# Kernel tuning notes

Hardware: AMD Instinct MI355X
Metric: run time of the kernel (lower is better)

The kernel has to match this reference:

```python
import jax, jax.numpy as jnp
import numpy as np

B, H, S, D = 2, 12, 2048, 64

def setup_inputs() -> dict:
    key = jax.random.key(0)
    kq, kk, kv = jax.random.split(key, 3)
    Q = jax.random.normal(kq, (B, H, S, D), dtype=jnp.float32)
    K = jax.random.normal(kk, (B, H, S, D), dtype=jnp.float32)
    V = jax.random.normal(kv, (B, H, S, D), dtype=jnp.float32)
    return {"Q": Q, "K": K, "V": V}

def reference(Q, K, V):
    # NOTE: original code scales by sqrt(Q.shape[-2]) (the sequence length),
    # not the head dim — reproduced faithfully.
    scale = 1.0 / np.sqrt(Q.shape[-2]).astype(np.float32)
    scores = jnp.einsum('bhqd,bhkd->bhqk', Q, K) * scale  # [B,H,S,S]
    attn = jax.nn.softmax(scores, axis=-1)
    context = jnp.einsum('bhqk,bhkd->bhqd', attn, V)      # [B,H,S,D]
    # torch .squeeze(-1) only removes the last dim if it is size 1; D=64 so no-op
    return context
```

## Files before the change

### kernel.cpp

```cpp
#include <hip/hip_runtime.h>
#include <hip/hip_bf16.h>
#include <math.h>
#include <stdint.h>

#define BATCH 2
#define NH 12
#define SEQ 2048
#define HD 64
#define TQ 64
#define TK 64
#define NHEADS (BATCH*NH)
#define NIT (SEQ / TK)

typedef short bf16x8 __attribute__((ext_vector_type(8)));
typedef float f32x4 __attribute__((ext_vector_type(4)));
typedef float f32x16 __attribute__((ext_vector_type(16)));
typedef unsigned short us4_t __attribute__((ext_vector_type(4)));
typedef unsigned short us8_t __attribute__((ext_vector_type(8)));
typedef unsigned int u32x4 __attribute__((ext_vector_type(4)));

#if __has_builtin(__builtin_amdgcn_exp2f)
#define EXP2F(x) __builtin_amdgcn_exp2f(x)
#else
#define EXP2F(x) exp2f(x)
#endif

static __device__ __forceinline__ unsigned short f2bf(float f) {
    unsigned int u = __float_as_uint(f);
    u += 0x7fffu + ((u >> 16) & 1u);
    return (unsigned short)(u >> 16);
}

static __device__ __forceinline__ unsigned int pack2bf(float a, float b) {
    __hip_bfloat162 v = __float22bfloat162_rn(float2{a, b});
    return *(unsigned int*)&v;
}

static __device__ __forceinline__ void async_cp16(const void* g, void* l) {
    __builtin_amdgcn_global_load_lds(
        (const __attribute__((address_space(1))) void*)g,
        (__attribute__((address_space(3))) void*)(uintptr_t)l,
        16, 0, 0);
}

static __device__ __forceinline__ int tile_off(int r, int c) {
    int rp  = r >> 1;
    int pos = (((r & 1) << 3) | c) ^ (rp & 15);
    return rp * 128 + pos * 8;
}

__global__ __launch_bounds__(256)
void prep_kv(const float* __restrict__ K, const float* __restrict__ V,
             unsigned short* __restrict__ Kb, unsigned short* __restrict__ Vtb) {
    __shared__ unsigned short T[64][66];
    const int bh = blockIdx.x >> 5;
    const int s0 = (blockIdx.x & 31) * 64;
    const int tid = threadIdx.x;
    const size_t off = ((size_t)bh * SEQ + s0) * HD;

    #pragma unroll
    for (int u = 0; u < 4; ++u) {
        int idx = u * 1024 + tid * 4;
        float4 a = *(const float4*)&K[off + idx];
        us4_t r4 = { f2bf(a.x), f2bf(a.y), f2bf(a.z), f2bf(a.w) };
        *(us4_t*)&Kb[off + idx] = r4;
    }
    #pragma unroll
    for (int u = 0; u < 4; ++u) {
        int idx = u * 1024 + tid * 4;
        int r = idx >> 6, col = idx & 63;
        float4 a = *(const float4*)&V[off + idx];
        *(unsigned int*)&T[r][col]     = pack2bf(a.x, a.y);
        *(unsigned int*)&T[r][col + 2] = pack2bf(a.z, a.w);
    }
    __syncthreads();
    unsigned short* Vdst = Vtb + (size_t)bh * HD * SEQ;
    const int g = tid & 7, dd = tid >> 3;
    #pragma unroll
    for (int h = 0; h < 2; ++h) {
        int d = dd + 32 * h;
        us8_t r8;
        #pragma unroll
        for (int j = 0; j < 8; ++j) {
            int src = ((g >> 1) << 4) + ((j >> 2) << 3) + ((g & 1) << 2) + (j & 3);
            r8[j] = T[src][d];
        }
        *(us8_t*)&Vdst[(size_t)d * SEQ + s0 + g * 8] = r8;
    }
}

__global__ __launch_bounds__(256, 3)
void fa_main(const float* __restrict__ Q,
             const unsigned short* __restrict__ Kb,
             const unsigned short* __restrict__ Vtb,
             float* __restrict__ O, float qs) {
    const int x  = blockIdx.x & 7;
    const int t  = blockIdx.x >> 3;
    const int bh = x + 8 * (t % 3);
    const int qt = t / 3;
    const int q0 = qt * TQ;

    __shared__ __align__(16) unsigned char SH[49664];
    float* Lsum = (float*)(SH + 49152);
    float* Linv = (float*)(SH + 49408);
    float* ORed = (float*)SH;
    unsigned short* QS = (unsigned short*)(SH + 32768);

    const int tid  = threadIdx.x;
    const int w    = tid >> 6;
    const int mt   = w >> 1;
    const int nt   = w & 1;
    const int lane = tid & 63;
    const int l31  = lane & 31;
    const int hi   = lane >> 5;

    const float*          Qh = Q   + ((size_t)bh * SEQ + q0) * HD;
    const unsigned short* Kh = Kb  + (size_t)bh * SEQ * HD;
    const unsigned short* Vh = Vtb + (size_t)bh * HD * SEQ;

    int rS[2], cS[2];
    #pragma unroll
    for (int i = 0; i < 2; ++i) {
        int rp = w * 8 + 4 * i + (lane >> 4);
        int lc = (lane & 15) ^ (rp & 15);
        rS[i] = 2 * rp + (lc >> 3);
        cS[i] = lc & 7;
    }
    const int dst0 = (w * 8 + 0) * 128, dst1 = (w * 8 + 4) * 128;
    const size_t kG0 = (size_t)rS[0] * HD  + cS[0] * 8;
    const size_t kG1 = (size_t)rS[1] * HD  + cS[1] * 8;
    const size_t vG0 = (size_t)rS[0] * SEQ + cS[0] * 8;
    const size_t vG1 = (size_t)rS[1] * SEQ + cS[1] * 8;

    {
        unsigned short* K0 = (unsigned short*)(SH);
        unsigned short* V0 = (unsigned short*)(SH + 8192);
        async_cp16(Kh + kG0, &K0[dst0]);
        async_cp16(Kh + kG1, &K0[dst1]);
        async_cp16(Vh + vG0, &V0[dst0]);
        async_cp16(Vh + vG1, &V0[dst1]);
    }
    #pragma unroll
    for (int u = 0; u < 4; ++u) {
        int idx = u * 1024 + tid * 4;
        int r = idx >> 6, col = idx & 63;
        float4 a = *(const float4*)&Qh[idx];
        uint2 pk = { pack2bf(a.x * qs, a.y * qs), pack2bf(a.z * qs, a.w * qs) };
        *(uint2*)&QS[tile_off(r, col >> 3) + (col & 7)] = pk;
    }
    __syncthreads();

    bf16x8 qf[4];
    #pragma unroll
    for (int s = 0; s < 4; ++s)
        qf[s] = *(const bf16x8*)&QS[tile_off(mt * 32 + l31, s * 2 + hi)];
    __syncthreads();

    {
        unsigned short* K1 = (unsigned short*)(SH + 16384);
        unsigned short* V1 = (unsigned short*)(SH + 16384 + 8192);
        async_cp16(Kh + (size_t)TK * HD + kG0, &K1[dst0]);
        async_cp16(Kh + (size_t)TK * HD + kG1, &K1[dst1]);
        async_cp16(Vh + (size_t)TK + vG0,      &V1[dst0]);
        async_cp16(Vh + (size_t)TK + vG1,      &V1[dst1]);
    }

    int kOffL[4], vOffL[2][2];
    #pragma unroll
    for (int s = 0; s < 4; ++s) kOffL[s] = tile_off(nt * 32 + l31, s * 2 + hi);
    #pragma unroll
    for (int dt = 0; dt < 2; ++dt)
        #pragma unroll
        for (int ks = 0; ks < 2; ++ks)
            vOffL[dt][ks] = tile_off(dt * 32 + l31, nt * 4 + ks * 2 + hi);

    f32x16 o[2];
    o[0] = (f32x16)(0.f);
    o[1] = (f32x16)(0.f);
    float lsum = 0.f;

    unsigned int b0 = 0, b1 = 16384, b2 = 32768;

    #pragma unroll 2
    for (int it = 0; it < NIT; ++it) {
        if (it == NIT - 1) { asm volatile("s_waitcnt vmcnt(0)" ::: "memory"); }
        else               { asm volatile("s_waitcnt vmcnt(4)" ::: "memory"); }
        __builtin_amdgcn_s_barrier();

        if (it + 2 < NIT) {
            const size_t kv = (size_t)(it + 2) * TK;
            unsigned short* Kn = (unsigned short*)(SH + b2);
            unsigned short* Vn = (unsigned short*)(SH + b2 + 8192);
            async_cp16(Kh + kv * HD + kG0, &Kn[dst0]);
            async_cp16(Kh + kv * HD + kG1, &Kn[dst1]);
            async_cp16(Vh + kv + vG0,      &Vn[dst0]);
            async_cp16(Vh + kv + vG1,      &Vn[dst1]);
        }
        const unsigned short* Ks = (const unsigned short*)(SH + b0);
        const unsigned short* Vs = (const unsigned short*)(SH + b0 + 8192);

        bf16x8 vf[2][2];
        #pragma unroll
        for (int dt = 0; dt < 2; ++dt)
            #pragma unroll
            for (int ks = 0; ks < 2; ++ks)
                vf[dt][ks] = *(const bf16x8*)&Vs[vOffL[dt][ks]];

        f32x16 sc = (f32x16)(0.f);
        __builtin_amdgcn_s_setprio(1);
        #pragma unroll
        for (int s = 0; s < 4; ++s) {
            bf16x8 kf = *(const bf16x8*)&Ks[kOffL[s]];
            sc = __builtin_amdgcn_mfma_f32_32x32x16_bf16(kf, qf[s], sc, 0, 0, 0);
        }
        __builtin_amdgcn_s_setprio(0);

        float e0[8], e1[8];
        #pragma unroll
        for (int r = 0; r < 8; ++r) e0[r] = EXP2F(sc[r]);
        union { u32x4 d; bf16x8 h; } pu0, pu1;
        pu0.d = (u32x4){ pack2bf(e0[0], e0[1]), pack2bf(e0[2], e0[3]),
                         pack2bf(e0[4], e0[5]), pack2bf(e0[6], e0[7]) };
        bf16x8 pf0 = pu0.h;
        __builtin_amdgcn_s_setprio(1);
        o[0] = __builtin_amdgcn_mfma_f32_32x32x16_bf16(pf0, vf[0][0], o[0], 0, 0, 0);
        o[1] = __builtin_amdgcn_mfma_f32_32x32x16_bf16(pf0, vf[1][0], o[1], 0, 0, 0);
        __builtin_amdgcn_s_setprio(0);

        #pragma unroll
        for (int r = 0; r < 8; ++r) e1[r] = EXP2F(sc[8 + r]);
        pu1.d = (u32x4){ pack2bf(e1[0], e1[1]), pack2bf(e1[2], e1[3]),
                         pack2bf(e1[4], e1[5]), pack2bf(e1[6], e1[7]) };
        bf16x8 pf1 = pu1.h;
        __builtin_amdgcn_s_setprio(1);
        o[0] = __builtin_amdgcn_mfma_f32_32x32x16_bf16(pf1, vf[0][1], o[0], 0, 0, 0);
        o[1] = __builtin_amdgcn_mfma_f32_32x32x16_bf16(pf1, vf[1][1], o[1], 0, 0, 0);
        __builtin_amdgcn_s_setprio(0);

        float t0 = ((e0[0] + e0[1]) + (e0[2] + e0[3]))
                 + ((e0[4] + e0[5]) + (e0[6] + e0[7]));
        float t1 = ((e1[0] + e1[1]) + (e1[2] + e1[3]))
                 + ((e1[4] + e1[5]) + (e1[6] + e1[7]));
        lsum += t0 + t1;

        unsigned int btmp = b0; b0 = b1; b1 = b2; b2 = btmp;
    }

    lsum += __shfl_xor(lsum, 32, 64);

    if (nt == 1) {
        if (lane < 32) Lsum[mt * 32 + lane] = lsum;
        #pragma unroll
        for (int dt = 0; dt < 2; ++dt) {
            const int d = dt * 32 + l31;
            #pragma unroll
            for (int g = 0; g < 4; ++g) {
                const int m0 = mt * 32 + 8 * g + 4 * hi;
                const int ph = (m0 >> 2) ^ (d & 15);
                float4 v = { o[dt][4*g+0], o[dt][4*g+1], o[dt][4*g+2], o[dt][4*g+3] };
                *(float4*)&ORed[d * 64 + ph * 4] = v;
            }
        }
    }
    __syncthreads();

    if (nt == 0) {
        float ltot = lsum + Lsum[mt * 32 + l31];
        if (lane < 32) Linv[mt * 32 + lane] = 1.0f / ltot;
        float* Oh = O + ((size_t)bh * SEQ + q0) * HD;
        #pragma unroll
        for (int dt = 0; dt < 2; ++dt) {
            const int d = dt * 32 + l31;
            #pragma unroll
            for (int g = 0; g < 4; ++g) {
                const int m0 = mt * 32 + 8 * g + 4 * hi;
                const int ph = (m0 >> 2) ^ (d & 15);
                float4 part = *(const float4*)&ORed[d * 64 + ph * 4];
                float4 inv4 = *(const float4*)&Linv[m0];
                const float* pp = (const float*)&part;
                const float* ii = (const float*)&inv4;
                #pragma unroll
                for (int j = 0; j < 4; ++j)
                    Oh[(size_t)(m0 + j) * HD + d] = (o[dt][4*g+j] + pp[j]) * ii[j];
            }
        }
    }
}

#define PAD 8
#define LSTR (HD + PAD)

__global__ __launch_bounds__(256)
void fa_fwd_fb(const float* __restrict__ Q, const float* __restrict__ K,
               const float* __restrict__ V, float* __restrict__ O) {
    const int x  = blockIdx.x & 7;
    const int t  = blockIdx.x >> 3;
    const int bh = x + 8 * (t % 3);
    const int qt = t / 3;
    const int q0 = qt * TQ;
    const long base = (long)bh * SEQ * HD;

    __shared__ unsigned short Qs[TQ][LSTR];
    __shared__ unsigned short Ks2[64][LSTR];
    __shared__ unsigned short Vt[HD][64 + PAD];
    __shared__ unsigned short Ps2[4][16][LSTR];

    const int tid  = threadIdx.x;
    const int wave = tid >> 6;
    const int lane = tid & 63;
    const int col  = lane & 15;
    const int quad = lane >> 4;
    const int m0   = wave * 16;

    #pragma unroll
    for (int i = 0; i < 4; ++i) {
        int idx = tid + 256 * i;
        int row = idx >> 4;
        int c4  = (idx & 15) * 4;
        float4 v = *(const float4*)&Q[base + (long)(q0 + row) * HD + c4];
        ushort4 b = { f2bf(v.x), f2bf(v.y), f2bf(v.z), f2bf(v.w) };
        *(ushort4*)&Qs[row][c4] = b;
    }
    __syncthreads();

    bf16x8 aq0 = *(const bf16x8*)&Qs[m0 + col][quad * 8];
    bf16x8 aq1 = *(const bf16x8*)&Qs[m0 + col][32 + quad * 8];

    f32x4 o0 = {0.f,0.f,0.f,0.f}, o1 = o0, o2 = o0, o3 = o0;
    float l[4] = {0.f, 0.f, 0.f, 0.f};
    const float scale = 0.022097086912079608f;

    for (int kv0 = 0; kv0 < SEQ; kv0 += 64) {
        __syncthreads();
        #pragma unroll
        for (int i = 0; i < 4; ++i) {
            int idx = tid + 256 * i;
            int row = idx >> 4;
            int c4  = (idx & 15) * 4;
            float4 kv = *(const float4*)&K[base + (long)(kv0 + row) * HD + c4];
            ushort4 kb = { f2bf(kv.x), f2bf(kv.y), f2bf(kv.z), f2bf(kv.w) };
            *(ushort4*)&Ks2[row][c4] = kb;
            float4 vv = *(const float4*)&V[base + (long)(kv0 + row) * HD + c4];
            Vt[c4 + 0][row] = f2bf(vv.x);
            Vt[c4 + 1][row] = f2bf(vv.y);
            Vt[c4 + 2][row] = f2bf(vv.z);
            Vt[c4 + 3][row] = f2bf(vv.w);
        }
        __syncthreads();

        f32x4 sc[4];
        #pragma unroll
        for (int n = 0; n < 4; ++n) {
            bf16x8 b0 = *(const bf16x8*)&Ks2[n * 16 + col][quad * 8];
            bf16x8 b1 = *(const bf16x8*)&Ks2[n * 16 + col][32 + quad * 8];
            f32x4 acc = {0.f,0.f,0.f,0.f};
            acc = __builtin_amdgcn_mfma_f32_16x16x32_bf16(aq0, b0, acc, 0, 0, 0);
            acc = __builtin_amdgcn_mfma_f32_16x16x32_bf16(aq1, b1, acc, 0, 0, 0);
            sc[n] = acc;
        }

        float tsum[4] = {0.f, 0.f, 0.f, 0.f};
        #pragma unroll
        for (int n = 0; n < 4; ++n) {
            #pragma unroll
            for (int r = 0; r < 4; ++r) {
                float p = __expf(sc[n][r] * scale);
                tsum[r] += p;
                Ps2[wave][quad * 4 + r][n * 16 + col] = f2bf(p);
            }
        }
        #pragma unroll
        for (int off = 1; off < 16; off <<= 1) {
            #pragma unroll
            for (int r = 0; r < 4; ++r) tsum[r] += __shfl_xor(tsum[r], off, 64);
        }
        #pragma unroll
        for (int r = 0; r < 4; ++r) l[r] += tsum[r];

        bf16x8 ap0 = *(const bf16x8*)&Ps2[wave][col][quad * 8];
        bf16x8 ap1 = *(const bf16x8*)&Ps2[wave][col][32 + quad * 8];
        #pragma unroll
        for (int n = 0; n < 4; ++n) {
            bf16x8 b0 = *(const bf16x8*)&Vt[n * 16 + col][quad * 8];
            bf16x8 b1 = *(const bf16x8*)&Vt[n * 16 + col][32 + quad * 8];
            f32x4* op = (n == 0) ? &o0 : (n == 1) ? &o1 : (n == 2) ? &o2 : &o3;
            *op = __builtin_amdgcn_mfma_f32_16x16x32_bf16(ap0, b0, *op, 0, 0, 0);
            *op = __builtin_amdgcn_mfma_f32_16x16x32_bf16(ap1, b1, *op, 0, 0, 0);
        }
    }

    float inv[4];
    #pragma unroll
    for (int r = 0; r < 4; ++r) inv[r] = 1.0f / l[r];
    #pragma unroll
    for (int r = 0; r < 4; ++r) {
        long row = base + (long)(q0 + m0 + quad * 4 + r) * HD;
        O[row +  0 + col] = o0[r] * inv[r];
        O[row + 16 + col] = o1[r] * inv[r];
        O[row + 32 + col] = o2[r] * inv[r];
        O[row + 48 + col] = o3[r] * inv[r];
    }
}

extern "C" void kernel_launch(void* const* d_in, const int* in_sizes, int n_in,
                              void* d_out, int out_size, void* d_ws, size_t ws_size,
                              hipStream_t stream) {
    const float* Q = (const float*)d_in[0];
    const float* K = (const float*)d_in[1];
    const float* V = (const float*)d_in[2];
    float* O = (float*)d_out;

    const size_t tensorElems = (size_t)NHEADS * SEQ * HD;
    const size_t need = 2 * tensorElems * sizeof(unsigned short);

    if (ws_size >= need) {
        unsigned short* Kb  = (unsigned short*)d_ws;
        unsigned short* Vtb = Kb + tensorElems;
        const float qs = (float)(1.4426950408889634 / sqrt(2048.0));
        prep_kv<<<dim3(NHEADS * (SEQ / 64)), dim3(256), 0, stream>>>(K, V, Kb, Vtb);
        fa_main<<<dim3(NHEADS * (SEQ / TQ)), dim3(256), 0, stream>>>(Q, Kb, Vtb, O, qs);
    } else {
        fa_fwd_fb<<<dim3(NHEADS * (SEQ / TQ)), dim3(256), 0, stream>>>(Q, K, V, O);
    }
}
```

Baseline: 117.5 us.

## Software-pipeline QK^T of next tile with softmax and PV of previous tile

```diff
diff --git a/kernel.cpp b/kernel.cpp
--- a/kernel.cpp
+++ b/kernel.cpp
@@ -179,10 +179,62 @@
     o[1] = (f32x16)(0.f);
     float lsum = 0.f;
 
+    auto FIN = [&](const f32x16& sp, const bf16x8 (&vp)[2][2]) {
+        float e0[8], e1[8];
+        #pragma unroll
+        for (int r = 0; r < 8; ++r) e0[r] = EXP2F(sp[r]);
+        #pragma unroll
+        for (int r = 0; r < 8; ++r) e1[r] = EXP2F(sp[8 + r]);
+        union { u32x4 d; bf16x8 h; } pu0, pu1;
+        pu0.d = (u32x4){ pack2bf(e0[0], e0[1]), pack2bf(e0[2], e0[3]),
+                         pack2bf(e0[4], e0[5]), pack2bf(e0[6], e0[7]) };
+        pu1.d = (u32x4){ pack2bf(e1[0], e1[1]), pack2bf(e1[2], e1[3]),
+                         pack2bf(e1[4], e1[5]), pack2bf(e1[6], e1[7]) };
+        bf16x8 pf0 = pu0.h, pf1 = pu1.h;
+        o[0] = __builtin_amdgcn_mfma_f32_32x32x16_bf16(pf0, vp[0][0], o[0], 0, 0, 0);
+        o[1] = __builtin_amdgcn_mfma_f32_32x32x16_bf16(pf0, vp[1][0], o[1], 0, 0, 0);
+        o[0] = __builtin_amdgcn_mfma_f32_32x32x16_bf16(pf1, vp[0][1], o[0], 0, 0, 0);
+        o[1] = __builtin_amdgcn_mfma_f32_32x32x16_bf16(pf1, vp[1][1], o[1], 0, 0, 0);
+        float t0 = ((e0[0] + e0[1]) + (e0[2] + e0[3]))
+                 + ((e0[4] + e0[5]) + (e0[6] + e0[7]));
+        float t1 = ((e1[0] + e1[1]) + (e1[2] + e1[3]))
+                 + ((e1[4] + e1[5]) + (e1[6] + e1[7]));
+        lsum += t0 + t1;
+    };
+
     unsigned int b0 = 0, b1 = 16384, b2 = 32768;
 
+    f32x16 scp;
+    bf16x8 vfp[2][2];
+
+    {
+        unsigned short* Kn = (unsigned short*)(SH + b2);
+        unsigned short* Vn = (unsigned short*)(SH + b2 + 8192);
+        async_cp16(Kh + (size_t)2 * TK * HD + kG0, &Kn[dst0]);
+        async_cp16(Kh + (size_t)2 * TK * HD + kG1, &Kn[dst1]);
+        async_cp16(Vh + (size_t)2 * TK + vG0,      &Vn[dst0]);
+        async_cp16(Vh + (size_t)2 * TK + vG1,      &Vn[dst1]);
+
+        const unsigned short* Ks = (const unsigned short*)(SH + b0);
+        const unsigned short* Vs = (const unsigned short*)(SH + b0 + 8192);
+        #pragma unroll
+        for (int dt = 0; dt < 2; ++dt)
+            #pragma unroll
+            for (int ks = 0; ks < 2; ++ks)
+                vfp[dt][ks] = *(const bf16x8*)&Vs[vOffL[dt][ks]];
+        f32x16 sc = (f32x16)(0.f);
+        #pragma unroll
+        for (int s = 0; s < 4; ++s) {
+            bf16x8 kf = *(const bf16x8*)&Ks[kOffL[s]];
+            sc = __builtin_amdgcn_mfma_f32_32x32x16_bf16(kf, qf[s], sc, 0, 0, 0);
+        }
+        scp = sc;
+        unsigned int btmp = b0; b0 = b1; b1 = b2; b2 = btmp;
+    }
+
     #pragma unroll 2
-    for (int it = 0; it < NIT; ++it) {
+    for (int it = 1; it < NIT; ++it) {
+        asm volatile("s_waitcnt lgkmcnt(0)" ::: "memory");
         if (it == NIT - 1) { asm volatile("s_waitcnt vmcnt(0)" ::: "memory"); }
         else               { asm volatile("s_waitcnt vmcnt(4)" ::: "memory"); }
         __builtin_amdgcn_s_barrier();
@@ -199,52 +251,32 @@
         const unsigned short* Ks = (const unsigned short*)(SH + b0);
         const unsigned short* Vs = (const unsigned short*)(SH + b0 + 8192);
 
-        bf16x8 vf[2][2];
+        bf16x8 vfc[2][2];
         #pragma unroll
         for (int dt = 0; dt < 2; ++dt)
             #pragma unroll
             for (int ks = 0; ks < 2; ++ks)
-                vf[dt][ks] = *(const bf16x8*)&Vs[vOffL[dt][ks]];
-
-        f32x16 sc = (f32x16)(0.f);
-        __builtin_amdgcn_s_setprio(1);
+                vfc[dt][ks] = *(const bf16x8*)&Vs[vOffL[dt][ks]];
+
+        f32x16 scc = (f32x16)(0.f);
         #pragma unroll
         for (int s = 0; s < 4; ++s) {
             bf16x8 kf = *(const bf16x8*)&Ks[kOffL[s]];
-            sc = __builtin_amdgcn_mfma_f32_32x32x16_bf16(kf, qf[s], sc, 0, 0, 0);
-        }
-        __builtin_amdgcn_s_setprio(0);
-
-        float e0[8], e1[8];
-        #pragma unroll
-        for (int r = 0; r < 8; ++r) e0[r] = EXP2F(sc[r]);
-        union { u32x4 d; bf16x8 h; } pu0, pu1;
-        pu0.d = (u32x4){ pack2bf(e0[0], e0[1]), pack2bf(e0[2], e0[3]),
-                         pack2bf(e0[4], e0[5]), pack2bf(e0[6], e0[7]) };
-        bf16x8 pf0 = pu0.h;
-        __builtin_amdgcn_s_setprio(1);
-        o[0] = __builtin_amdgcn_mfma_f32_32x32x16_bf16(pf0, vf[0][0], o[0], 0, 0, 0);
-        o[1] = __builtin_amdgcn_mfma_f32_32x32x16_bf16(pf0, vf[1][0], o[1], 0, 0, 0);
-        __builtin_amdgcn_s_setprio(0);
-
-        #pragma unroll
-        for (int r = 0; r < 8; ++r) e1[r] = EXP2F(sc[8 + r]);
-        pu1.d = (u32x4){ pack2bf(e1[0], e1[1]), pack2bf(e1[2], e1[3]),
-                         pack2bf(e1[4], e1[5]), pack2bf(e1[6], e1[7]) };
-        bf16x8 pf1 = pu1.h;
-        __builtin_amdgcn_s_setprio(1);
-        o[0] = __builtin_amdgcn_mfma_f32_32x32x16_bf16(pf1, vf[0][1], o[0], 0, 0, 0);
-        o[1] = __builtin_amdgcn_mfma_f32_32x32x16_bf16(pf1, vf[1][1], o[1], 0, 0, 0);
-        __builtin_amdgcn_s_setprio(0);
-
-        float t0 = ((e0[0] + e0[1]) + (e0[2] + e0[3]))
-                 + ((e0[4] + e0[5]) + (e0[6] + e0[7]));
-        float t1 = ((e1[0] + e1[1]) + (e1[2] + e1[3]))
-                 + ((e1[4] + e1[5]) + (e1[6] + e1[7]));
-        lsum += t0 + t1;
+            scc = __builtin_amdgcn_mfma_f32_32x32x16_bf16(kf, qf[s], scc, 0, 0, 0);
+        }
+        FIN(scp, vfp);
+
+        scp = scc;
+        #pragma unroll
+        for (int dt = 0; dt < 2; ++dt)
+            #pragma unroll
+            for (int ks = 0; ks < 2; ++ks)
+                vfp[dt][ks] = vfc[dt][ks];
 
         unsigned int btmp = b0; b0 = b1; b1 = b2; b2 = btmp;
     }
+
+    FIN(scp, vfp);
 
     lsum += __shfl_xor(lsum, 32, 64);
 
```

New measurement: 115.8 us. No clear change (-1.5%).
